# Performance work log

Hardware: AMD Instinct MI355X
Metric: run time of the kernel (lower is better)

Reference implementation:

```python
import jax, jax.numpy as jnp
import numpy as np

B, L, H = 4, 512, 768
S, R = 100, 100          # num spans, num relations
E = 25                   # size embedding dim
MAXLEN = 100             # max entity length (size embedding vocab)
NE, NR = 10, 6           # entity / relation type counts
NEG = jnp.float32(-1e20)


def _span_masks(key, batch, n, seqlen, max_len):
    k1, k2 = jax.random.split(key)
    starts = jax.random.randint(k1, (batch, n), 0, seqlen - max_len)
    lens = jax.random.randint(k2, (batch, n), 1, max_len)
    pos = jnp.arange(seqlen)
    m = (pos[None, None, :] >= starts[..., None]) & (pos[None, None, :] < (starts + lens)[..., None])
    return m.astype(jnp.int32)  # (batch, n, seqlen), contiguous 0/1 spans


def setup_inputs() -> dict:
    key = jax.random.key(0)
    ks = jax.random.split(key, 8)
    hidden_states = jax.random.normal(ks[0], (B, L, H), dtype=jnp.float32)
    entity_masks = _span_masks(ks[1], B, S, L, 20)            # span len < MAXLEN
    relation_context_masks = _span_masks(ks[2], B, R, L, 50)  # context len < MAXLEN
    relations = jax.random.randint(ks[3], (B, R, 2), 0, S)
    size_emb = jax.random.normal(ks[4], (MAXLEN, E), dtype=jnp.float32) * 0.02
    w_span = jax.random.normal(ks[5], (E + H, NE), dtype=jnp.float32) * 0.02
    b_span = jnp.zeros((NE,), dtype=jnp.float32)
    w_rel = jax.random.normal(ks[6], (2 * E + 3 * H, NR), dtype=jnp.float32) * 0.02
    b_rel = jnp.zeros((NR,), dtype=jnp.float32)
    return {
        'hidden_states': hidden_states,
        'entity_masks': entity_masks,
        'relations': relations,
        'relation_context_masks': relation_context_masks,
        'size_emb': size_emb,
        'w_span': w_span,
        'b_span': b_span,
        'w_rel': w_rel,
        'b_rel': b_rel,
    }


def _masked_max(hidden, masks):
    # hidden: (B, L, H); masks: (B, N, L) 0/1 -> (B, N, H) max over masked positions
    # Matches torch: h.unsqueeze(1)*m then masked_fill(m==0, -1e20), max over L
    masked = jnp.where(masks[..., None] != 0, hidden[:, None, :, :], NEG)
    return jnp.max(masked, axis=-2)


def reference(hidden_states, entity_masks, relations, relation_context_masks,
              size_emb, w_span, b_span, w_rel, b_rel):
    # entity sizes -> size embedding lookup
    entity_sizes = size_emb[entity_masks.sum(-1)]                     # (B, S, E)

    # entity span max-pool + classify
    entities = _masked_max(hidden_states, entity_masks)               # (B, S, H)
    entity_reprs = jnp.concatenate([entities, entity_sizes], axis=-1)
    entity_logits = entity_reprs @ w_span + b_span                    # (B, S, NE)

    # relation context max-pool
    rel_ctx = _masked_max(hidden_states, relation_context_masks)      # (B, R, H)

    # gather entity pairs
    b, r = relations.shape[:2]
    rel_flat = relations.reshape(b, -1)                               # (B, 2R)
    pairs = jnp.take_along_axis(entities, rel_flat[:, :, None], axis=1).reshape(b, r, -1)
    pair_sizes = jnp.take_along_axis(entity_sizes, rel_flat[:, :, None], axis=1).reshape(b, r, -1)

    rel_reprs = jnp.concatenate([rel_ctx, pairs, pair_sizes], axis=-1)
    relation_logits = rel_reprs @ w_rel + b_rel                       # (B, R, NR)
    return entity_logits, relation_logits
```

## Files before the change

kernel.cpp:

```cpp
#include <hip/hip_runtime.h>

#define B 4
#define L 512
#define H 768
#define S 100
#define R 100
#define E 25
#define NE 10
#define NR 6
#define NEGF (-1e20f)

__global__ __launch_bounds__(256) void pool_kernel(
    const float* __restrict__ hidden,
    const int*   __restrict__ emask,
    const int*   __restrict__ cmask,
    const float* __restrict__ size_emb,
    const float* __restrict__ w_span,
    const float* __restrict__ b_span,
    float* __restrict__ entities,
    float* __restrict__ sizes,
    float* __restrict__ rel_ctx,
    float* __restrict__ ent_logits)
{
    const int idx = blockIdx.x;
    const int b = idx / (S + R);
    const int j = idx % (S + R);
    const bool is_span = (j < S);

    __shared__ int   poss[L];
    __shared__ int   s_cnt;
    __shared__ float s_red[4][NE];

    if (threadIdx.x == 0) s_cnt = 0;
    __syncthreads();

    const int* mrow = is_span ? (emask + (size_t)(b * S + j) * L)
                              : (cmask + (size_t)(b * R + (j - S)) * L);
    for (int l = (int)threadIdx.x; l < L; l += 256) {
        if (mrow[l] != 0) {
            int p = atomicAdd(&s_cnt, 1);
            poss[p] = l;
        }
    }
    __syncthreads();
    const int n = s_cnt;

    const int h0 = threadIdx.x, h1 = threadIdx.x + 256, h2 = threadIdx.x + 512;
    float mv0 = NEGF, mv1 = NEGF, mv2 = NEGF;
    const float* hb = hidden + (size_t)b * L * H;
    for (int i = 0; i < n; ++i) {
        const float* hp = hb + (size_t)poss[i] * H;
        mv0 = fmaxf(mv0, hp[h0]);
        mv1 = fmaxf(mv1, hp[h1]);
        mv2 = fmaxf(mv2, hp[h2]);
    }

    if (!is_span) {
        const int r = j - S;
        float* orow = rel_ctx + (size_t)(b * R + r) * H;
        orow[h0] = mv0; orow[h1] = mv1; orow[h2] = mv2;
        return;
    }

    const int s = j;
    float* erow = entities + (size_t)(b * S + s) * H;
    erow[h0] = mv0; erow[h1] = mv1; erow[h2] = mv2;

    const float* srow_src = size_emb + (size_t)n * E;
    float* srow = sizes + (size_t)(b * S + s) * E;
    if (threadIdx.x < E) srow[threadIdx.x] = srow_src[threadIdx.x];

    float p[NE];
    #pragma unroll
    for (int o = 0; o < NE; ++o)
        p[o] = mv0 * w_span[(size_t)h0 * NE + o]
             + mv1 * w_span[(size_t)h1 * NE + o]
             + mv2 * w_span[(size_t)h2 * NE + o];

    #pragma unroll
    for (int o = 0; o < NE; ++o) {
        float v = p[o];
        for (int off = 32; off > 0; off >>= 1) v += __shfl_down(v, off, 64);
        p[o] = v;
    }
    const int wave = threadIdx.x >> 6;
    const int lane = threadIdx.x & 63;
    if (lane == 0) {
        #pragma unroll
        for (int o = 0; o < NE; ++o) s_red[wave][o] = p[o];
    }
    __syncthreads();
    if (threadIdx.x < NE) {
        const int o = threadIdx.x;
        float v = s_red[0][o] + s_red[1][o] + s_red[2][o] + s_red[3][o];
        #pragma unroll
        for (int e = 0; e < E; ++e)
            v += srow_src[e] * w_span[(size_t)(H + e) * NE + o];
        v += b_span[o];
        ent_logits[(size_t)(b * S + s) * NE + o] = v;
    }
}

__global__ __launch_bounds__(256) void rel_kernel(
    const float* __restrict__ entities,
    const float* __restrict__ sizes,
    const float* __restrict__ rel_ctx,
    const int*   __restrict__ relations,
    const float* __restrict__ w_rel,
    const float* __restrict__ b_rel,
    float* __restrict__ rel_logits)
{
    const int idx = blockIdx.x;
    const int b = idx / R;
    const int r = idx % R;
    const int head = relations[(size_t)(b * R + r) * 2 + 0];
    const int tail = relations[(size_t)(b * R + r) * 2 + 1];

    const float* ctx = rel_ctx  + (size_t)(b * R + r)    * H;
    const float* eh  = entities + (size_t)(b * S + head) * H;
    const float* et  = entities + (size_t)(b * S + tail) * H;
    const float* sh  = sizes    + (size_t)(b * S + head) * E;
    const float* st  = sizes    + (size_t)(b * S + tail) * E;

    const int D = 3 * H + 2 * E;
    float p[NR] = {0.f, 0.f, 0.f, 0.f, 0.f, 0.f};
    for (int i = (int)threadIdx.x; i < D; i += 256) {
        float x;
        if      (i < H)         x = ctx[i];
        else if (i < 2 * H)     x = eh[i - H];
        else if (i < 3 * H)     x = et[i - 2 * H];
        else if (i < 3 * H + E) x = sh[i - 3 * H];
        else                    x = st[i - 3 * H - E];
        const float* wr = w_rel + (size_t)i * NR;
        #pragma unroll
        for (int o = 0; o < NR; ++o) p[o] += x * wr[o];
    }

    __shared__ float s_red[4][NR];
    #pragma unroll
    for (int o = 0; o < NR; ++o) {
        float v = p[o];
        for (int off = 32; off > 0; off >>= 1) v += __shfl_down(v, off, 64);
        p[o] = v;
    }
    const int wave = threadIdx.x >> 6;
    const int lane = threadIdx.x & 63;
    if (lane == 0) {
        #pragma unroll
        for (int o = 0; o < NR; ++o) s_red[wave][o] = p[o];
    }
    __syncthreads();
    if (threadIdx.x < NR) {
        const int o = threadIdx.x;
        float v = s_red[0][o] + s_red[1][o] + s_red[2][o] + s_red[3][o] + b_rel[o];
        rel_logits[(size_t)(b * R + r) * NR + o] = v;
    }
}

extern "C" void kernel_launch(void* const* d_in, const int* in_sizes, int n_in,
                              void* d_out, int out_size, void* d_ws, size_t ws_size,
                              hipStream_t stream) {
    const float* hidden    = (const float*)d_in[0];
    const int*   emask     = (const int*)  d_in[1];
    const int*   relations = (const int*)  d_in[2];
    const int*   cmask     = (const int*)  d_in[3];
    const float* size_emb  = (const float*)d_in[4];
    const float* w_span    = (const float*)d_in[5];
    const float* b_span    = (const float*)d_in[6];
    const float* w_rel     = (const float*)d_in[7];
    const float* b_rel     = (const float*)d_in[8];

    float* out        = (float*)d_out;
    float* ent_logits = out;
    float* rel_logits = out + B * S * NE;

    float* ws       = (float*)d_ws;
    float* entities = ws;
    float* sizes    = entities + (size_t)B * S * H;
    float* rel_ctx  = sizes + (size_t)B * S * E;

    pool_kernel<<<B * (S + R), 256, 0, stream>>>(
        hidden, emask, cmask, size_emb, w_span, b_span,
        entities, sizes, rel_ctx, ent_logits);

    rel_kernel<<<B * R, 256, 0, stream>>>(
        entities, sizes, rel_ctx, relations, w_rel, b_rel, rel_logits);
}
```

Baseline: 87.04 us.

## Fuse pooling and relation classifier into one kernel using contiguous-span masks

```diff
diff --git a/kernel.cpp b/kernel.cpp
--- a/kernel.cpp
+++ b/kernel.cpp
@@ -10,150 +10,160 @@
 #define NR 6
 #define NEGF (-1e20f)
 
-__global__ __launch_bounds__(256) void pool_kernel(
+__device__ __forceinline__ void mask_stats_partial(
+    const int* __restrict__ mrow, int t, int wave, int lane,
+    int (*sc)[4], int (*sm)[4], int k)
+{
+    int c = 0, mn = L;
+    #pragma unroll
+    for (int i = 0; i < 2; ++i) {
+        const int l = t + i * 256;
+        const int m = mrow[l];
+        c += (m != 0);
+        if (m != 0 && l < mn) mn = l;
+    }
+    for (int off = 32; off > 0; off >>= 1) {
+        c += __shfl_down(c, off, 64);
+        mn = min(mn, __shfl_down(mn, off, 64));
+    }
+    if (lane == 0) { sc[k][wave] = c; sm[k][wave] = mn; }
+}
+
+__device__ __forceinline__ void span_pool(
+    const float* __restrict__ hb, int start, int n,
+    int h0, int h1, int h2, float& mv0, float& mv1, float& mv2)
+{
+    mv0 = NEGF; mv1 = NEGF; mv2 = NEGF;
+    const float* hp = hb + (size_t)start * H;
+    for (int i = 0; i < n; ++i, hp += H) {
+        mv0 = fmaxf(mv0, hp[h0]);
+        mv1 = fmaxf(mv1, hp[h1]);
+        mv2 = fmaxf(mv2, hp[h2]);
+    }
+}
+
+__global__ __launch_bounds__(256) void spert_fused_kernel(
     const float* __restrict__ hidden,
     const int*   __restrict__ emask,
+    const int*   __restrict__ relations,
     const int*   __restrict__ cmask,
     const float* __restrict__ size_emb,
     const float* __restrict__ w_span,
     const float* __restrict__ b_span,
-    float* __restrict__ entities,
-    float* __restrict__ sizes,
-    float* __restrict__ rel_ctx,
-    float* __restrict__ ent_logits)
-{
-    const int idx = blockIdx.x;
-    const int b = idx / (S + R);
-    const int j = idx % (S + R);
-    const bool is_span = (j < S);
-
-    __shared__ int   poss[L];
-    __shared__ int   s_cnt;
-    __shared__ float s_red[4][NE];
-
-    if (threadIdx.x == 0) s_cnt = 0;
-    __syncthreads();
-
-    const int* mrow = is_span ? (emask + (size_t)(b * S + j) * L)
-                              : (cmask + (size_t)(b * R + (j - S)) * L);
-    for (int l = (int)threadIdx.x; l < L; l += 256) {
-        if (mrow[l] != 0) {
-            int p = atomicAdd(&s_cnt, 1);
-            poss[p] = l;
-        }
-    }
-    __syncthreads();
-    const int n = s_cnt;
-
-    const int h0 = threadIdx.x, h1 = threadIdx.x + 256, h2 = threadIdx.x + 512;
-    float mv0 = NEGF, mv1 = NEGF, mv2 = NEGF;
-    const float* hb = hidden + (size_t)b * L * H;
-    for (int i = 0; i < n; ++i) {
-        const float* hp = hb + (size_t)poss[i] * H;
-        mv0 = fmaxf(mv0, hp[h0]);
-        mv1 = fmaxf(mv1, hp[h1]);
-        mv2 = fmaxf(mv2, hp[h2]);
-    }
-
-    if (!is_span) {
-        const int r = j - S;
-        float* orow = rel_ctx + (size_t)(b * R + r) * H;
-        orow[h0] = mv0; orow[h1] = mv1; orow[h2] = mv2;
-        return;
-    }
-
-    const int s = j;
-    float* erow = entities + (size_t)(b * S + s) * H;
-    erow[h0] = mv0; erow[h1] = mv1; erow[h2] = mv2;
-
-    const float* srow_src = size_emb + (size_t)n * E;
-    float* srow = sizes + (size_t)(b * S + s) * E;
-    if (threadIdx.x < E) srow[threadIdx.x] = srow_src[threadIdx.x];
-
-    float p[NE];
-    #pragma unroll
-    for (int o = 0; o < NE; ++o)
-        p[o] = mv0 * w_span[(size_t)h0 * NE + o]
-             + mv1 * w_span[(size_t)h1 * NE + o]
-             + mv2 * w_span[(size_t)h2 * NE + o];
-
-    #pragma unroll
-    for (int o = 0; o < NE; ++o) {
-        float v = p[o];
-        for (int off = 32; off > 0; off >>= 1) v += __shfl_down(v, off, 64);
-        p[o] = v;
-    }
-    const int wave = threadIdx.x >> 6;
-    const int lane = threadIdx.x & 63;
-    if (lane == 0) {
-        #pragma unroll
-        for (int o = 0; o < NE; ++o) s_red[wave][o] = p[o];
-    }
-    __syncthreads();
-    if (threadIdx.x < NE) {
-        const int o = threadIdx.x;
-        float v = s_red[0][o] + s_red[1][o] + s_red[2][o] + s_red[3][o];
-        #pragma unroll
-        for (int e = 0; e < E; ++e)
-            v += srow_src[e] * w_span[(size_t)(H + e) * NE + o];
-        v += b_span[o];
-        ent_logits[(size_t)(b * S + s) * NE + o] = v;
-    }
-}
-
-__global__ __launch_bounds__(256) void rel_kernel(
-    const float* __restrict__ entities,
-    const float* __restrict__ sizes,
-    const float* __restrict__ rel_ctx,
-    const int*   __restrict__ relations,
     const float* __restrict__ w_rel,
     const float* __restrict__ b_rel,
+    float* __restrict__ ent_logits,
     float* __restrict__ rel_logits)
 {
-    const int idx = blockIdx.x;
-    const int b = idx / R;
-    const int r = idx % R;
-    const int head = relations[(size_t)(b * R + r) * 2 + 0];
-    const int tail = relations[(size_t)(b * R + r) * 2 + 1];
+    const int idx  = blockIdx.x;
+    const int b    = idx / (S + R);
+    const int j    = idx % (S + R);
+    const int t    = threadIdx.x;
+    const int wave = t >> 6;
+    const int lane = t & 63;
+    const int h0 = t, h1 = t + 256, h2 = t + 512;
 
-    const float* ctx = rel_ctx  + (size_t)(b * R + r)    * H;
-    const float* eh  = entities + (size_t)(b * S + head) * H;
-    const float* et  = entities + (size_t)(b * S + tail) * H;
-    const float* sh  = sizes    + (size_t)(b * S + head) * E;
-    const float* st  = sizes    + (size_t)(b * S + tail) * E;
+    __shared__ int   sc[3][4], sm[3][4];
+    __shared__ float sred[4][NE];
 
-    const int D = 3 * H + 2 * E;
-    float p[NR] = {0.f, 0.f, 0.f, 0.f, 0.f, 0.f};
-    for (int i = (int)threadIdx.x; i < D; i += 256) {
-        float x;
-        if      (i < H)         x = ctx[i];
-        else if (i < 2 * H)     x = eh[i - H];
-        else if (i < 3 * H)     x = et[i - 2 * H];
-        else if (i < 3 * H + E) x = sh[i - 3 * H];
-        else                    x = st[i - 3 * H - E];
-        const float* wr = w_rel + (size_t)i * NR;
+    const float* hb = hidden + (size_t)b * L * H;
+
+    if (j < S) {
+        const int* mrow = emask + (size_t)(b * S + j) * L;
+        mask_stats_partial(mrow, t, wave, lane, sc, sm, 0);
+        __syncthreads();
+        const int n     = sc[0][0] + sc[0][1] + sc[0][2] + sc[0][3];
+        const int start = min(min(sm[0][0], sm[0][1]), min(sm[0][2], sm[0][3]));
+
+        float mv0, mv1, mv2;
+        span_pool(hb, start, n, h0, h1, h2, mv0, mv1, mv2);
+
+        float p[NE];
         #pragma unroll
-        for (int o = 0; o < NR; ++o) p[o] += x * wr[o];
-    }
+        for (int o = 0; o < NE; ++o)
+            p[o] = mv0 * w_span[(size_t)h0 * NE + o]
+                 + mv1 * w_span[(size_t)h1 * NE + o]
+                 + mv2 * w_span[(size_t)h2 * NE + o];
+        if (t < E) {
+            const float sz = size_emb[(size_t)n * E + t];
+            #pragma unroll
+            for (int o = 0; o < NE; ++o) p[o] += sz * w_span[(size_t)(H + t) * NE + o];
+        }
+        #pragma unroll
+        for (int o = 0; o < NE; ++o) {
+            float v = p[o];
+            for (int off = 32; off > 0; off >>= 1) v += __shfl_down(v, off, 64);
+            p[o] = v;
+        }
+        if (lane == 0) {
+            #pragma unroll
+            for (int o = 0; o < NE; ++o) sred[wave][o] = p[o];
+        }
+        __syncthreads();
+        if (t < NE) {
+            const float v = sred[0][t] + sred[1][t] + sred[2][t] + sred[3][t] + b_span[t];
+            ent_logits[(size_t)(b * S + j) * NE + t] = v;
+        }
+    } else {
+        const int r    = j - S;
+        const int head = relations[(size_t)(b * R + r) * 2 + 0];
+        const int tail = relations[(size_t)(b * R + r) * 2 + 1];
 
-    __shared__ float s_red[4][NR];
-    #pragma unroll
-    for (int o = 0; o < NR; ++o) {
-        float v = p[o];
-        for (int off = 32; off > 0; off >>= 1) v += __shfl_down(v, off, 64);
-        p[o] = v;
-    }
-    const int wave = threadIdx.x >> 6;
-    const int lane = threadIdx.x & 63;
-    if (lane == 0) {
+        mask_stats_partial(cmask + (size_t)(b * R + r)    * L, t, wave, lane, sc, sm, 0);
+        mask_stats_partial(emask + (size_t)(b * S + head) * L, t, wave, lane, sc, sm, 1);
+        mask_stats_partial(emask + (size_t)(b * S + tail) * L, t, wave, lane, sc, sm, 2);
+        __syncthreads();
+
+        int n[3], st[3];
         #pragma unroll
-        for (int o = 0; o < NR; ++o) s_red[wave][o] = p[o];
-    }
-    __syncthreads();
-    if (threadIdx.x < NR) {
-        const int o = threadIdx.x;
-        float v = s_red[0][o] + s_red[1][o] + s_red[2][o] + s_red[3][o] + b_rel[o];
-        rel_logits[(size_t)(b * R + r) * NR + o] = v;
+        for (int k = 0; k < 3; ++k) {
+            n[k]  = sc[k][0] + sc[k][1] + sc[k][2] + sc[k][3];
+            st[k] = min(min(sm[k][0], sm[k][1]), min(sm[k][2], sm[k][3]));
+        }
+
+        float mv[3][3];
+        #pragma unroll
+        for (int k = 0; k < 3; ++k)
+            span_pool(hb, st[k], n[k], h0, h1, h2, mv[k][0], mv[k][1], mv[k][2]);
+
+        float p[NR];
+        #pragma unroll
+        for (int o = 0; o < NR; ++o)
+            p[o] = mv[0][0] * w_rel[(size_t) h0          * NR + o]
+                 + mv[0][1] * w_rel[(size_t) h1          * NR + o]
+                 + mv[0][2] * w_rel[(size_t) h2          * NR + o]
+                 + mv[1][0] * w_rel[(size_t)(H + h0)     * NR + o]
+                 + mv[1][1] * w_rel[(size_t)(H + h1)     * NR + o]
+                 + mv[1][2] * w_rel[(size_t)(H + h2)     * NR + o]
+                 + mv[2][0] * w_rel[(size_t)(2 * H + h0) * NR + o]
+                 + mv[2][1] * w_rel[(size_t)(2 * H + h1) * NR + o]
+                 + mv[2][2] * w_rel[(size_t)(2 * H + h2) * NR + o];
+        if (t < E) {
+            const float sz = size_emb[(size_t)n[1] * E + t];
+            #pragma unroll
+            for (int o = 0; o < NR; ++o) p[o] += sz * w_rel[(size_t)(3 * H + t) * NR + o];
+        } else if (t >= 32 && t < 32 + E) {
+            const int e = t - 32;
+            const float sz = size_emb[(size_t)n[2] * E + e];
+            #pragma unroll
+            for (int o = 0; o < NR; ++o) p[o] += sz * w_rel[(size_t)(3 * H + E + e) * NR + o];
+        }
+
+        #pragma unroll
+        for (int o = 0; o < NR; ++o) {
+            float v = p[o];
+            for (int off = 32; off > 0; off >>= 1) v += __shfl_down(v, off, 64);
+            p[o] = v;
+        }
+        if (lane == 0) {
+            #pragma unroll
+            for (int o = 0; o < NR; ++o) sred[wave][o] = p[o];
+        }
+        __syncthreads();
+        if (t < NR) {
+            const float v = sred[0][t] + sred[1][t] + sred[2][t] + sred[3][t] + b_rel[t];
+            rel_logits[(size_t)(b * R + r) * NR + t] = v;
+        }
     }
 }
 
@@ -174,15 +184,7 @@
     float* ent_logits = out;
     float* rel_logits = out + B * S * NE;
 
-    float* ws       = (float*)d_ws;
-    float* entities = ws;
-    float* sizes    = entities + (size_t)B * S * H;
-    float* rel_ctx  = sizes + (size_t)B * S * E;
-
-    pool_kernel<<<B * (S + R), 256, 0, stream>>>(
-        hidden, emask, cmask, size_emb, w_span, b_span,
-        entities, sizes, rel_ctx, ent_logits);
-
-    rel_kernel<<<B * R, 256, 0, stream>>>(
-        entities, sizes, rel_ctx, relations, w_rel, b_rel, rel_logits);
+    spert_fused_kernel<<<B * (S + R), 256, 0, stream>>>(
+        hidden, emask, relations, cmask, size_emb,
+        w_span, b_span, w_rel, b_rel, ent_logits, rel_logits);
 }
```

Result: slower. 94.65 us (+8.7%).
